# Optimization experiments

Hardware: AMD Instinct MI355X
Metric: run time of the kernel (lower is better)

## Reference

```python
import jax, jax.numpy as jnp
import numpy as np

B, C, H, W = 2, 64, 320, 640
TF = 16
HIDDEN = 48
HALF = 2
G = 8
D = 2 * HALF + 1
IN_CH = 2 * C + TF + 4 + G * D  # 164


def _sample_x(f, xs):
    # f: (B,C,H,W); xs: (B,H,W) absolute x sample coords.
    # Equivalent to F.grid_sample(align_corners=True, padding_mode='border')
    # with gy hitting exact integer rows -> pure 1D bilinear along W with border clamp.
    Wd = f.shape[-1]
    xs = jnp.clip(xs, 0.0, Wd - 1)
    x0 = jnp.floor(xs)
    w = (xs - x0)[:, None]                      # (B,1,H,W)
    i0 = x0.astype(jnp.int32)[:, None]          # (B,1,H,W)
    i1 = jnp.minimum(i0 + 1, Wd - 1)
    g0 = jnp.take_along_axis(f, jnp.broadcast_to(i0, f.shape), axis=3)
    g1 = jnp.take_along_axis(f, jnp.broadcast_to(i1, f.shape), axis=3)
    return g0 * (1.0 - w) + g1 * w


def _warp(fR, d):
    xx = jnp.arange(fR.shape[-1], dtype=fR.dtype)
    return _sample_x(fR, xx[None, None, :] - d[:, 0])


def _corr(fL, fR, d):
    b, c, h, w = fL.shape
    cg = c // G
    xx = jnp.arange(w, dtype=fL.dtype)
    fL_g = fL.reshape(b, G, cg, h, w)
    outs = []
    for i in range(D):  # small fixed D=5 loop over disparity offsets
        off = float(i - HALF)
        fR_w = _sample_x(fR, xx[None, None, :] - (d[:, 0] + off))
        outs.append((fL_g * fR_w.reshape(b, G, cg, h, w)).mean(axis=2))
    return jnp.stack(outs, axis=2).reshape(b, G * D, h, w)


def _conv(x, w, pad):
    return jax.lax.conv_general_dilated(x, w, (1, 1), ((pad, pad), (pad, pad)),
                                        dimension_numbers=('NCHW', 'OIHW', 'NCHW'))


def _gn(x, gamma, beta, groups=8, eps=1e-5):
    b, c, h, w = x.shape
    xg = x.reshape(b, groups, -1)
    m = xg.mean(axis=2, keepdims=True)
    v = ((xg - m) ** 2).mean(axis=2, keepdims=True)
    xg = (xg - m) * jax.lax.rsqrt(v + eps)
    return xg.reshape(b, c, h, w) * gamma[None, :, None, None] + beta[None, :, None, None]


def _head(h, w, b):
    return _conv(h, w, 0) + b[None, :, None, None]


def setup_inputs():
    key = jax.random.key(0)
    ks = jax.random.split(key, 32)
    inp = {}
    inp['d'] = jax.random.uniform(ks[0], (B, 1, H, W)) * 64.0
    inp['sx'] = jax.random.normal(ks[1], (B, 1, H, W)) * 0.1
    inp['sy'] = jax.random.normal(ks[2], (B, 1, H, W)) * 0.1
    inp['feat'] = jax.random.normal(ks[3], (B, TF, H, W))
    inp['conf'] = jax.random.uniform(ks[4], (B, 1, H, W))
    inp['fL'] = jax.random.normal(ks[5], (B, C, H, W))
    inp['fR'] = jax.random.normal(ks[6], (B, C, H, W))

    def cw(k, o, i, s):
        return jax.random.normal(k, (o, i, s, s)) * (1.0 / np.sqrt(i * s * s))

    inp['conv1_w'] = cw(ks[7], HIDDEN, IN_CH, 3)
    inp['conv2_w'] = cw(ks[8], HIDDEN, HIDDEN, 3)
    inp['conv3_w'] = cw(ks[9], HIDDEN, HIDDEN, 3)
    for j, nm in enumerate(['gn1', 'gn2', 'gn3']):
        inp[nm + '_g'] = 1.0 + 0.1 * jax.random.normal(ks[10 + 2 * j], (HIDDEN,))
        inp[nm + '_b'] = 0.1 * jax.random.normal(ks[11 + 2 * j], (HIDDEN,))
    inp['hd_w'] = cw(ks[16], 1, HIDDEN, 1); inp['hd_b'] = 0.01 * jax.random.normal(ks[17], (1,))
    inp['hsx_w'] = cw(ks[18], 1, HIDDEN, 1); inp['hsx_b'] = 0.01 * jax.random.normal(ks[19], (1,))
    inp['hsy_w'] = cw(ks[20], 1, HIDDEN, 1); inp['hsy_b'] = 0.01 * jax.random.normal(ks[21], (1,))
    inp['hc_w'] = cw(ks[22], 1, HIDDEN, 1); inp['hc_b'] = 0.01 * jax.random.normal(ks[23], (1,))
    inp['hf_w'] = cw(ks[24], TF, HIDDEN, 1); inp['hf_b'] = 0.01 * jax.random.normal(ks[25], (TF,))
    return inp


def reference(d, sx, sy, feat, conf, fL, fR,
              conv1_w, conv2_w, conv3_w,
              gn1_g, gn1_b, gn2_g, gn2_b, gn3_g, gn3_b,
              hd_w, hd_b, hsx_w, hsx_b, hsy_w, hsy_b, hc_w, hc_b, hf_w, hf_b):
    fR_w = _warp(fR, d)                               # standard warp (slope_aware off)
    cost = _corr(fL, fR, d)                           # (B, G*D, H, W)
    x = jnp.concatenate([fL, fR_w, feat, d, sx, sy, conf, cost], axis=1)
    h = jax.nn.silu(_gn(_conv(x, conv1_w, 1), gn1_g, gn1_b))
    h = jax.nn.silu(_gn(_conv(h, conv2_w, 1), gn2_g, gn2_b))
    h = jax.nn.silu(_gn(_conv(h, conv3_w, 1), gn3_g, gn3_b))
    d_out = jax.nn.softplus(_head(h, hd_w, hd_b) + d)  # gate == 1.0
    sx_out = sx + _head(h, hsx_w, hsx_b) * 0.1
    sy_out = sy + _head(h, hsy_w, hsy_b) * 0.1
    conf_out = jax.nn.sigmoid(_head(h, hc_w, hc_b) + 2.0 * conf - 1.0)
    feat_out = feat + _head(h, hf_w, hf_b)
    return (d_out, sx_out, sy_out, feat_out, conf_out)
```

## Files before the change

### kernel.cpp

```cpp
#include <hip/hip_runtime.h>
#include <hip/hip_bf16.h>

typedef __hip_bfloat16 bf16;
typedef unsigned short u16;
typedef short v8s __attribute__((ext_vector_type(8)));
typedef u16   v8u __attribute__((ext_vector_type(8)));
typedef float v4f __attribute__((ext_vector_type(4)));

#define Hd 320
#define Wd 640
#define HWP (Hd*Wd)
#define Bn 2
#define NCH1 188
#define HID 48
#define NBHW (Bn*HWP)
#define CP 40
#define NPIX 324
#define NSLAB 13

static __device__ __forceinline__ float b2f(bf16 v){ return __bfloat162float(v); }
static __device__ __forceinline__ bf16  f2b(float v){ return __float2bfloat16(v); }
static __device__ __forceinline__ u16 f2u(float v){ bf16 t = f2b(v); return *reinterpret_cast<u16*>(&t); }
static __device__ __forceinline__ float u2f(u16 u){ return __uint_as_float(((unsigned)u) << 16); }

template<typename T> static __device__ __forceinline__ float ld(const T* p, long i);
template<> __device__ __forceinline__ float ld<bf16>(const bf16* p, long i){ return b2f(p[i]); }
template<> __device__ __forceinline__ float ld<float>(const float* p, long i){ return p[i]; }
template<typename T> static __device__ __forceinline__ void stv(T* p, long i, float v);
template<> __device__ __forceinline__ void stv<bf16>(bf16* p, long i, float v){ p[i] = f2b(v); }
template<> __device__ __forceinline__ void stv<float>(float* p, long i, float v){ p[i] = v; }
template<typename T> struct want_flag;
template<> struct want_flag<bf16>  { static const int v = 0; };
template<> struct want_flag<float> { static const int v = 1; };

__global__ void probe_k(const u16* __restrict__ dq, int* __restrict__ flag)
{
  __shared__ int cnt;
  if (threadIdx.x == 0) cnt = 0;
  __syncthreads();
  int bad = 0;
  for (int i = threadIdx.x; i < 2048; i += 256) {
    float v = __uint_as_float(((unsigned)dq[2*i]) << 16);
    if (!(fabsf(v) <= 65.f)) bad++;
  }
  atomicAdd(&cnt, bad);
  __syncthreads();
  if (threadIdx.x == 0) *flag = (cnt > 64) ? 1 : 0;
}

static __device__ __forceinline__ int pack2orig(int p)
{
  if (p < 128) return p;
  if (p < 168) { int idx = p - 128; int i5 = idx >> 3, g = idx & 7; return 148 + g*5 + i5; }
  if (p < 184) return 128 + (p - 168);
  if (p < 188) return 144 + (p - 184);
  return -1;
}

template<typename T>
__global__ void wconv_k(const int* __restrict__ flag,
                        const T* __restrict__ c1, const T* __restrict__ c2,
                        const T* __restrict__ c3,
                        const T* __restrict__ hdw, const T* __restrict__ hdb,
                        const T* __restrict__ hsxw, const T* __restrict__ hsxb,
                        const T* __restrict__ hsyw, const T* __restrict__ hsyb,
                        const T* __restrict__ hcw,  const T* __restrict__ hcb,
                        const T* __restrict__ hfw,  const T* __restrict__ hfb,
                        u16* __restrict__ wf1, u16* __restrict__ wf2,
                        u16* __restrict__ wf3, float* __restrict__ wh,
                        float* __restrict__ bh)
{
  if (*flag != want_flag<T>::v) return;
  int stride = gridDim.x * blockDim.x;
  int t0 = blockIdx.x * blockDim.x + threadIdx.x;
  const int N1 = 6*9*3*64*8;
  for (int idx = t0; idx < N1; idx += stride) {
    int j = idx & 7; int lane = (idx >> 3) & 63; int rest = idx >> 9;
    int nt = rest % 3; rest /= 3; int tap = rest % 9; int chunk = rest / 9;
    int oc = nt*16 + (lane & 15);
    int cin = pack2orig(chunk*32 + (lane >> 4)*8 + j);
    float v = (cin >= 0) ? ld(c1, ((long)oc*NCH1 + cin)*9 + tap) : 0.f;
    wf1[idx] = f2u(v);
  }
  const int N2 = 2*9*3*64*8;
  for (int idx = t0; idx < N2; idx += stride) {
    int j = idx & 7; int lane = (idx >> 3) & 63; int rest = idx >> 9;
    int nt = rest % 3; rest /= 3; int tap = rest % 9; int chunk = rest / 9;
    int oc = nt*16 + (lane & 15);
    int cin = chunk*32 + (lane >> 4)*8 + j;
    float v2 = 0.f, v3 = 0.f;
    if (cin < HID) {
      v2 = ld(c2, ((long)oc*HID + cin)*9 + tap);
      v3 = ld(c3, ((long)oc*HID + cin)*9 + tap);
    }
    wf2[idx] = f2u(v2);
    wf3[idx] = f2u(v3);
  }
  for (int i = t0; i < HID; i += stride) {
    wh[0*HID + i] = ld(hdw, i);
    wh[1*HID + i] = ld(hsxw, i);
    wh[2*HID + i] = ld(hsyw, i);
    wh[3*HID + i] = ld(hcw, i);
  }
  for (int i = t0; i < 16*HID; i += stride) wh[4*HID + i] = ld(hfw, i);
  if (t0 == 0) {
    bh[0] = ld(hdb,0); bh[1] = ld(hsxb,0); bh[2] = ld(hsyb,0); bh[3] = ld(hcb,0);
    for (int j = 0; j < 16; ++j) bh[4+j] = ld(hfb, j);
  }
}

template<typename T>
__global__ __launch_bounds__(640) void build_x_k(
    const int* __restrict__ flag, int b,
    const T* __restrict__ dP,
    const T* __restrict__ fL, const T* __restrict__ fR,
    u16* __restrict__ xpk)
{
  if (*flag != want_flag<T>::v) return;
  __shared__ float rowR[8][Wd];
  int y = blockIdx.x;
  int x = threadIdx.x;
  long rowoff = (long)y*Wd;
  long pix = rowoff + x;
  float dval = ld(dP, (long)b*HWP + pix);
  float base = (float)x - dval;
  float i0f = floorf(base);
  float w = base - i0f;
  int i0b = (int)i0f;
  int idx0 = min(max(i0b - 2, 0), Wd-1);
  int idx1 = min(max(i0b - 1, 0), Wd-1);
  int idx2 = min(max(i0b    , 0), Wd-1);
  int idx3 = min(max(i0b + 1, 0), Wd-1);
  int idx4 = min(max(i0b + 2, 0), Wd-1);
  int idx5 = min(max(i0b + 3, 0), Wd-1);
  v8u cv0, cv1, cv2, cv3, cv4;

  #pragma unroll
  for (int g = 0; g < 8; ++g) {
    __syncthreads();
    #pragma unroll
    for (int cc = 0; cc < 8; ++cc)
      rowR[cc][x] = ld(fR, ((long)(b*64 + g*8 + cc))*HWP + rowoff + x);
    __syncthreads();
    v8u fwv;
    float a0=0.f, a1=0.f, a2=0.f, a3=0.f, a4=0.f;
    #pragma unroll
    for (int cc = 0; cc < 8; ++cc) {
      float fl = ld(fL, ((long)(b*64 + g*8 + cc))*HWP + pix);
      const float* rr = rowR[cc];
      float r0 = rr[idx0], r1 = rr[idx1], r2 = rr[idx2];
      float r3 = rr[idx3], r4 = rr[idx4], r5 = rr[idx5];
      float s0 = r4 + w*(r5 - r4);
      float s1 = r3 + w*(r4 - r3);
      float s2v = r2 + w*(r3 - r2);
      float s3 = r1 + w*(r2 - r1);
      float s4 = r0 + w*(r1 - r0);
      a0 += fl*s0; a1 += fl*s1; a2 += fl*s2v; a3 += fl*s3; a4 += fl*s4;
      fwv[cc] = f2u(s2v);
    }
    __builtin_nontemporal_store(fwv, (v8u*)&xpk[((long)g*HWP + pix)*8]);
    cv0[g] = f2u(a0*0.125f);
    cv1[g] = f2u(a1*0.125f);
    cv2[g] = f2u(a2*0.125f);
    cv3[g] = f2u(a3*0.125f);
    cv4[g] = f2u(a4*0.125f);
  }
  __builtin_nontemporal_store(cv0, (v8u*)&xpk[((long) 8*HWP + pix)*8]);
  __builtin_nontemporal_store(cv1, (v8u*)&xpk[((long) 9*HWP + pix)*8]);
  __builtin_nontemporal_store(cv2, (v8u*)&xpk[((long)10*HWP + pix)*8]);
  __builtin_nontemporal_store(cv3, (v8u*)&xpk[((long)11*HWP + pix)*8]);
  __builtin_nontemporal_store(cv4, (v8u*)&xpk[((long)12*HWP + pix)*8]);
}

static __device__ __forceinline__ void conv_epilogue(
    v4f (*acc)[3], u16* lds, float (*sred)[2], u16* out48,
    float* st, int b, int x0, int y0, int tid)
{
  int lane = tid & 63, wave = tid >> 6;
  #pragma unroll
  for (int nt = 0; nt < 3; ++nt) {
    float s = 0.f, s2 = 0.f;
    #pragma unroll
    for (int mi = 0; mi < 4; ++mi)
      #pragma unroll
      for (int r = 0; r < 4; ++r) { float v = acc[mi][nt][r]; s += v; s2 += v*v; }
    s  += __shfl_xor(s, 16);  s2 += __shfl_xor(s2, 16);
    s  += __shfl_xor(s, 32);  s2 += __shfl_xor(s2, 32);
    if (lane < 16) {
      int g = (nt*16 + lane) / 6;
      atomicAdd(&sred[g][0], s);
      atomicAdd(&sred[g][1], s2);
    }
  }
  __syncthreads();
  #pragma unroll
  for (int mi = 0; mi < 4; ++mi) {
    int py = wave*4 + mi;
    #pragma unroll
    for (int nt = 0; nt < 3; ++nt) {
      int oc = nt*16 + (lane & 15);
      #pragma unroll
      for (int r = 0; r < 4; ++r) {
        int px = (lane >> 4)*4 + r;
        lds[oc*270 + py*16 + px] = f2u(acc[mi][nt][r]);
      }
    }
  }
  __syncthreads();
  {
    int pix = tid;
    long base = ((long)(y0 + (pix>>4))*Wd + (x0 + (pix&15)))*HID;
    #pragma unroll
    for (int k = 0; k < 6; ++k) {
      v8u o;
      #pragma unroll
      for (int jj = 0; jj < 8; ++jj) o[jj] = lds[(k*8 + jj)*270 + pix];
      *(v8u*)&out48[base + k*8] = o;
    }
  }
  if (tid < 16) atomicAdd(&st[(b*8 + (tid>>1))*2 + (tid&1)], sred[tid>>1][tid&1]);
}

template<typename T>
__global__ __launch_bounds__(256) void conv1m_k(
    const int* __restrict__ flag, int b,
    const T* __restrict__ fL, const T* __restrict__ featP,
    const T* __restrict__ dP, const T* __restrict__ sxP, const T* __restrict__ syP,
    const T* __restrict__ confP,
    const u16* __restrict__ xpk, const u16* __restrict__ wfrag,
    u16* __restrict__ out48, float* __restrict__ st)
{
  if (*flag != want_flag<T>::v) return;
  __shared__ __attribute__((aligned(16))) u16 lds[12960];
  __shared__ float sred[8][2];
  int x0 = blockIdx.x*16, y0 = blockIdx.y*16;
  int tid = threadIdx.x, lane = tid & 63, wave = tid >> 6;
  if (tid < 16) ((float*)sred)[tid] = 0.f;
  const T* fLb = fL + (long)b*64*HWP;
  v4f acc[4][3];
  #pragma unroll
  for (int mi = 0; mi < 4; ++mi)
    #pragma unroll
    for (int nt = 0; nt < 3; ++nt) acc[mi][nt] = (v4f){0.f,0.f,0.f,0.f};

  for (int ch = 0; ch < 6; ++ch) {
    __syncthreads();
    for (int j = tid; j < 4*NPIX; j += 256) {
      int pix = j >> 2, q = j & 3;
      int r = pix / 18, cl = pix - r*18;
      int gy = y0 - 1 + r, gx = x0 - 1 + cl;
      bool inb = ((unsigned)gy < Hd) & ((unsigned)gx < Wd);
      long rowb = (long)gy*Wd + gx;
      v8u vals = {0,0,0,0,0,0,0,0};
      if (inb) {
        if (ch < 2) {
          int c0 = ch*32 + q*8;
          #pragma unroll
          for (int jj = 0; jj < 8; ++jj)
            vals[jj] = f2u(ld(fLb, (long)(c0+jj)*HWP + rowb));
        } else if (ch < 4) {
          vals = *(const v8u*)&xpk[((long)((ch-2)*4 + q)*HWP + rowb)*8];
        } else if (ch == 4) {
          vals = *(const v8u*)&xpk[((long)(8 + q)*HWP + rowb)*8];
        } else {
          if (q == 0) {
            vals = *(const v8u*)&xpk[((long)12*HWP + rowb)*8];
          } else if (q < 3) {
            #pragma unroll
            for (int jj = 0; jj < 8; ++jj)
              vals[jj] = f2u(ld(featP, ((long)(b*16 + (q-1)*8 + jj))*HWP + rowb));
          } else {
            vals[0] = f2u(ld(dP,   (long)b*HWP + rowb));
            vals[1] = f2u(ld(sxP,  (long)b*HWP + rowb));
            vals[2] = f2u(ld(syP,  (long)b*HWP + rowb));
            vals[3] = f2u(ld(confP,(long)b*HWP + rowb));
          }
        }
      }
      *(v8u*)&lds[pix*CP + q*8] = vals;
    }
    __syncthreads();
    #pragma unroll
    for (int tap = 0; tap < 9; ++tap) {
      int dr = tap / 3, dc = tap - dr*3;
      v8s bf0 = *(const v8s*)&wfrag[((((ch*9+tap)*3 + 0)*64 + lane) << 3)];
      v8s bf1 = *(const v8s*)&wfrag[((((ch*9+tap)*3 + 1)*64 + lane) << 3)];
      v8s bf2 = *(const v8s*)&wfrag[((((ch*9+tap)*3 + 2)*64 + lane) << 3)];
      #pragma unroll
      for (int mi = 0; mi < 4; ++mi) {
        int py = wave*4 + mi;
        const v8s a = *(const v8s*)&lds[((py+dr)*18 + (lane&15) + dc)*CP + (lane>>4)*8];
        acc[mi][0] = __builtin_amdgcn_mfma_f32_16x16x32_bf16(a, bf0, acc[mi][0], 0, 0, 0);
        acc[mi][1] = __builtin_amdgcn_mfma_f32_16x16x32_bf16(a, bf1, acc[mi][1], 0, 0, 0);
        acc[mi][2] = __builtin_amdgcn_mfma_f32_16x16x32_bf16(a, bf2, acc[mi][2], 0, 0, 0);
      }
    }
  }
  __syncthreads();
  conv_epilogue(acc, lds, sred, out48, st, b, x0, y0, tid);
}

template<typename T>
__global__ __launch_bounds__(256) void convHm_k(
    const int* __restrict__ flag, int b,
    const u16* __restrict__ in48, const u16* __restrict__ wfrag,
    const float* __restrict__ stats, const T* __restrict__ gamma,
    const T* __restrict__ beta, u16* __restrict__ out48, float* __restrict__ st)
{
  if (*flag != want_flag<T>::v) return;
  __shared__ __attribute__((aligned(16))) u16 lds[12960];
  __shared__ float sred[8][2];
  __shared__ float sc[HID], of[HID];
  int x0 = blockIdx.x*16, y0 = blockIdx.y*16;
  int tid = threadIdx.x, lane = tid & 63, wave = tid >> 6;
  if (tid < 16) ((float*)sred)[tid] = 0.f;
  if (tid < HID) {
    int g = tid / 6;
    const float inv_n = 1.f / (6.f * HWP);
    float s  = stats[(b*8+g)*2+0];
    float s2 = stats[(b*8+g)*2+1];
    float m  = s * inv_n;
    float var = s2 * inv_n - m*m;
    float rs = rsqrtf(fmaxf(var, 0.f) + 1e-5f);
    float gm = ld(gamma, tid), bt = ld(beta, tid);
    sc[tid] = rs * gm;
    of[tid] = bt - m * rs * gm;
  }
  v4f acc[4][3];
  #pragma unroll
  for (int mi = 0; mi < 4; ++mi)
    #pragma unroll
    for (int nt = 0; nt < 3; ++nt) acc[mi][nt] = (v4f){0.f,0.f,0.f,0.f};

  for (int ch = 0; ch < 2; ++ch) {
    int cb = ch*32;
    __syncthreads();
    for (int j = tid; j < 4*NPIX; j += 256) {
      int pix = j >> 2, q = j & 3;
      int r = pix / 18, cl = pix - r*18;
      int gy = y0 - 1 + r, gx = x0 - 1 + cl;
      int c0 = cb + q*8;
      v8u vals = {0,0,0,0,0,0,0,0};
      if ((((unsigned)gy < Hd) & ((unsigned)gx < Wd)) && c0 < HID) {
        v8u raw = *(const v8u*)&in48[((long)gy*Wd + gx)*HID + c0];
        #pragma unroll
        for (int jj = 0; jj < 8; ++jj) {
          float v = u2f(raw[jj]) * sc[c0+jj] + of[c0+jj];
          vals[jj] = f2u(v / (1.f + __expf(-v)));
        }
      }
      *(v8u*)&lds[pix*CP + q*8] = vals;
    }
    __syncthreads();
    #pragma unroll
    for (int tap = 0; tap < 9; ++tap) {
      int dr = tap / 3, dc = tap - dr*3;
      v8s bf0 = *(const v8s*)&wfrag[((((ch*9+tap)*3 + 0)*64 + lane) << 3)];
      v8s bf1 = *(const v8s*)&wfrag[((((ch*9+tap)*3 + 1)*64 + lane) << 3)];
      v8s bf2 = *(const v8s*)&wfrag[((((ch*9+tap)*3 + 2)*64 + lane) << 3)];
      #pragma unroll
      for (int mi = 0; mi < 4; ++mi) {
        int py = wave*4 + mi;
        const v8s a = *(const v8s*)&lds[((py+dr)*18 + (lane&15) + dc)*CP + (lane>>4)*8];
        acc[mi][0] = __builtin_amdgcn_mfma_f32_16x16x32_bf16(a, bf0, acc[mi][0], 0, 0, 0);
        acc[mi][1] = __builtin_amdgcn_mfma_f32_16x16x32_bf16(a, bf1, acc[mi][1], 0, 0, 0);
        acc[mi][2] = __builtin_amdgcn_mfma_f32_16x16x32_bf16(a, bf2, acc[mi][2], 0, 0, 0);
      }
    }
  }
  __syncthreads();
  conv_epilogue(acc, lds, sred, out48, st, b, x0, y0, tid);
}

template<typename T>
__global__ __launch_bounds__(256) void heads_k(
    const int* __restrict__ flag, int b,
    const u16* __restrict__ h48, const float* __restrict__ st,
    const T* __restrict__ gamma, const T* __restrict__ beta,
    const float* __restrict__ wh, const float* __restrict__ bh,
    const T* __restrict__ dP, const T* __restrict__ sxP, const T* __restrict__ syP,
    const T* __restrict__ featP, const T* __restrict__ confP,
    T* __restrict__ out)
{
  if (*flag != want_flag<T>::v) return;
  __shared__ float sc[HID], of[HID];
  int p = blockIdx.x * 256 + threadIdx.x;
  long idx = (long)b*HWP + p;
  if (threadIdx.x < HID) {
    int c = threadIdx.x;
    int g = c / 6;
    const float inv_n = 1.f / (6.f * HWP);
    float s  = st[(b*8+g)*2+0];
    float s2 = st[(b*8+g)*2+1];
    float m  = s * inv_n;
    float var = s2 * inv_n - m*m;
    float rs = rsqrtf(fmaxf(var, 0.f) + 1e-5f);
    float gm = ld(gamma, c), bt = ld(beta, c);
    sc[c] = rs * gm;
    of[c] = bt - m * rs * gm;
  }
  __syncthreads();
  float hv[HID];
  #pragma unroll
  for (int k = 0; k < 6; ++k) {
    v8u h8 = *(const v8u*)&h48[(long)p*HID + k*8];
    #pragma unroll
    for (int jj = 0; jj < 8; ++jj) {
      int c = k*8 + jj;
      float v = u2f(h8[jj]) * sc[c] + of[c];
      hv[c] = v / (1.f + __expf(-v));
    }
  }
  float dot[20];
  #pragma unroll
  for (int r = 0; r < 20; ++r) {
    float a = bh[r];
    #pragma unroll
    for (int c = 0; c < HID; ++c) a += wh[r*HID + c] * hv[c];
    dot[r] = a;
  }
  float dval = ld(dP, idx);
  float xd = dot[0] + dval;
  float sp = fmaxf(xd, 0.f) + log1pf(__expf(-fabsf(xd)));
  stv(out, idx, sp);
  stv(out, NBHW + idx,    ld(sxP, idx) + 0.1f*dot[1]);
  stv(out, 2L*NBHW + idx, ld(syP, idx) + 0.1f*dot[2]);
  float cf = dot[3] + 2.f*ld(confP, idx) - 1.f;
  stv(out, 19L*NBHW + idx, 1.f/(1.f + __expf(-cf)));
  #pragma unroll
  for (int r = 0; r < 16; ++r) {
    long fi = ((long)(b*16 + r))*HWP + p;
    stv(out, 3L*NBHW + fi, ld(featP, fi) + dot[4+r]);
  }
}

extern "C" void kernel_launch(void* const* d_in, const int* in_sizes, int n_in,
                              void* d_out, int out_size, void* d_ws, size_t ws_size,
                              hipStream_t stream)
{
  char* ws = (char*)d_ws;
  size_t off = 0;
  u16* xpk = (u16*)(ws + off); off += (size_t)NSLAB*HWP*8*sizeof(u16);
  u16* h1  = (u16*)(ws + off); off += (size_t)HID*HWP*sizeof(u16);
  u16* wf1 = (u16*)(ws + off); off += (size_t)6*9*3*64*8*sizeof(u16);
  u16* wf2 = (u16*)(ws + off); off += (size_t)2*9*3*64*8*sizeof(u16);
  u16* wf3 = (u16*)(ws + off); off += (size_t)2*9*3*64*8*sizeof(u16);
  float* wh = (float*)(ws + off); off += (size_t)20*HID*sizeof(float);
  float* bh = (float*)(ws + off); off += 32*sizeof(float);
  float* st = (float*)(ws + off); off += 96*sizeof(float);
  int* flag = (int*)(ws + off);   off += sizeof(int);
  u16* h2 = xpk;
  u16* h3 = h1;

  hipMemsetAsync(st, 0, 96*sizeof(float), stream);
  probe_k<<<1, 256, 0, stream>>>((const u16*)d_in[0], flag);

  dim3 cgrid(Wd/16, Hd/16, 1);

  #define LAUNCH_ALL(T) do { \
    const T* dP    = (const T*)d_in[0]; \
    const T* sxP   = (const T*)d_in[1]; \
    const T* syP   = (const T*)d_in[2]; \
    const T* featP = (const T*)d_in[3]; \
    const T* confP = (const T*)d_in[4]; \
    const T* fL    = (const T*)d_in[5]; \
    const T* fR    = (const T*)d_in[6]; \
    wconv_k<T><<<320, 256, 0, stream>>>(flag, (const T*)d_in[7], (const T*)d_in[8], \
        (const T*)d_in[9], (const T*)d_in[16], (const T*)d_in[17], (const T*)d_in[18], \
        (const T*)d_in[19], (const T*)d_in[20], (const T*)d_in[21], (const T*)d_in[22], \
        (const T*)d_in[23], (const T*)d_in[24], (const T*)d_in[25], wf1, wf2, wf3, wh, bh); \
    for (int b = 0; b < Bn; ++b) { \
      build_x_k<T><<<Hd, 640, 0, stream>>>(flag, b, dP, fL, fR, xpk); \
      conv1m_k<T><<<cgrid, 256, 0, stream>>>(flag, b, fL, featP, dP, sxP, syP, confP, xpk, wf1, h1, st + 0); \
      convHm_k<T><<<cgrid, 256, 0, stream>>>(flag, b, h1, wf2, st + 0,  (const T*)d_in[10], (const T*)d_in[11], h2, st + 32); \
      convHm_k<T><<<cgrid, 256, 0, stream>>>(flag, b, h2, wf3, st + 32, (const T*)d_in[12], (const T*)d_in[13], h3, st + 64); \
      heads_k<T><<<HWP/256, 256, 0, stream>>>(flag, b, h3, st + 64, (const T*)d_in[14], (const T*)d_in[15], \
          wh, bh, dP, sxP, syP, featP, confP, (T*)d_out); \
    } \
  } while (0)

  LAUNCH_ALL(bf16);
  LAUNCH_ALL(float);
  #undef LAUNCH_ALL
}
```

Measured before the change: 879.8 us.

## Pack fL into xpk slabs and register-prefetch next channel chunk in convs

build_x_k now also writes fL as packed bf16 slabs (NSLAB grows to 21), so conv1 reads only packed 8-channel vectors instead of eight strided planar loads per pixel. Both conv kernels restructure the staging loop so the next channel chunk's global loads are issued into registers before the MFMA loop on the current chunk, then written to LDS afterward. This overlaps global latency with compute at the cost of extra registers, an extra slab of writes in build_x, and additional barriers.

```diff
diff --git a/kernel.cpp b/kernel.cpp
--- a/kernel.cpp
+++ b/kernel.cpp
@@ -16,7 +16,7 @@
 #define NBHW (Bn*HWP)
 #define CP 40
 #define NPIX 324
-#define NSLAB 13
+#define NSLAB 21
 
 static __device__ __forceinline__ float b2f(bf16 v){ return __bfloat162float(v); }
 static __device__ __forceinline__ bf16  f2b(float v){ return __float2bfloat16(v); }
@@ -142,11 +142,12 @@
     for (int cc = 0; cc < 8; ++cc)
       rowR[cc][x] = ld(fR, ((long)(b*64 + g*8 + cc))*HWP + rowoff + x);
     __syncthreads();
-    v8u fwv;
+    v8u flv, fwv;
     float a0=0.f, a1=0.f, a2=0.f, a3=0.f, a4=0.f;
     #pragma unroll
     for (int cc = 0; cc < 8; ++cc) {
       float fl = ld(fL, ((long)(b*64 + g*8 + cc))*HWP + pix);
+      flv[cc] = f2u(fl);
       const float* rr = rowR[cc];
       float r0 = rr[idx0], r1 = rr[idx1], r2 = rr[idx2];
       float r3 = rr[idx3], r4 = rr[idx4], r5 = rr[idx5];
@@ -158,18 +159,19 @@
       a0 += fl*s0; a1 += fl*s1; a2 += fl*s2v; a3 += fl*s3; a4 += fl*s4;
       fwv[cc] = f2u(s2v);
     }
-    __builtin_nontemporal_store(fwv, (v8u*)&xpk[((long)g*HWP + pix)*8]);
+    __builtin_nontemporal_store(flv, (v8u*)&xpk[((long)g*HWP + pix)*8]);
+    __builtin_nontemporal_store(fwv, (v8u*)&xpk[((long)(8 + g)*HWP + pix)*8]);
     cv0[g] = f2u(a0*0.125f);
     cv1[g] = f2u(a1*0.125f);
     cv2[g] = f2u(a2*0.125f);
     cv3[g] = f2u(a3*0.125f);
     cv4[g] = f2u(a4*0.125f);
   }
-  __builtin_nontemporal_store(cv0, (v8u*)&xpk[((long) 8*HWP + pix)*8]);
-  __builtin_nontemporal_store(cv1, (v8u*)&xpk[((long) 9*HWP + pix)*8]);
-  __builtin_nontemporal_store(cv2, (v8u*)&xpk[((long)10*HWP + pix)*8]);
-  __builtin_nontemporal_store(cv3, (v8u*)&xpk[((long)11*HWP + pix)*8]);
-  __builtin_nontemporal_store(cv4, (v8u*)&xpk[((long)12*HWP + pix)*8]);
+  __builtin_nontemporal_store(cv0, (v8u*)&xpk[((long)16*HWP + pix)*8]);
+  __builtin_nontemporal_store(cv1, (v8u*)&xpk[((long)17*HWP + pix)*8]);
+  __builtin_nontemporal_store(cv2, (v8u*)&xpk[((long)18*HWP + pix)*8]);
+  __builtin_nontemporal_store(cv3, (v8u*)&xpk[((long)19*HWP + pix)*8]);
+  __builtin_nontemporal_store(cv4, (v8u*)&xpk[((long)20*HWP + pix)*8]);
 }
 
 static __device__ __forceinline__ void conv_epilogue(
@@ -224,7 +226,7 @@
 template<typename T>
 __global__ __launch_bounds__(256) void conv1m_k(
     const int* __restrict__ flag, int b,
-    const T* __restrict__ fL, const T* __restrict__ featP,
+    const T* __restrict__ featP,
     const T* __restrict__ dP, const T* __restrict__ sxP, const T* __restrict__ syP,
     const T* __restrict__ confP,
     const u16* __restrict__ xpk, const u16* __restrict__ wfrag,
@@ -236,50 +238,69 @@
   int x0 = blockIdx.x*16, y0 = blockIdx.y*16;
   int tid = threadIdx.x, lane = tid & 63, wave = tid >> 6;
   if (tid < 16) ((float*)sred)[tid] = 0.f;
-  const T* fLb = fL + (long)b*64*HWP;
   v4f acc[4][3];
   #pragma unroll
   for (int mi = 0; mi < 4; ++mi)
     #pragma unroll
     for (int nt = 0; nt < 3; ++nt) acc[mi][nt] = (v4f){0.f,0.f,0.f,0.f};
 
-  for (int ch = 0; ch < 6; ++ch) {
-    __syncthreads();
-    for (int j = tid; j < 4*NPIX; j += 256) {
+  #pragma unroll
+  for (int k = 0; k < 6; ++k) {
+    int j = tid + k*256;
+    if (j < 4*NPIX) {
       int pix = j >> 2, q = j & 3;
       int r = pix / 18, cl = pix - r*18;
       int gy = y0 - 1 + r, gx = x0 - 1 + cl;
-      bool inb = ((unsigned)gy < Hd) & ((unsigned)gx < Wd);
-      long rowb = (long)gy*Wd + gx;
       v8u vals = {0,0,0,0,0,0,0,0};
-      if (inb) {
-        if (ch < 2) {
-          int c0 = ch*32 + q*8;
-          #pragma unroll
-          for (int jj = 0; jj < 8; ++jj)
-            vals[jj] = f2u(ld(fLb, (long)(c0+jj)*HWP + rowb));
-        } else if (ch < 4) {
-          vals = *(const v8u*)&xpk[((long)((ch-2)*4 + q)*HWP + rowb)*8];
-        } else if (ch == 4) {
-          vals = *(const v8u*)&xpk[((long)(8 + q)*HWP + rowb)*8];
-        } else {
-          if (q == 0) {
-            vals = *(const v8u*)&xpk[((long)12*HWP + rowb)*8];
-          } else if (q < 3) {
-            #pragma unroll
-            for (int jj = 0; jj < 8; ++jj)
-              vals[jj] = f2u(ld(featP, ((long)(b*16 + (q-1)*8 + jj))*HWP + rowb));
-          } else {
-            vals[0] = f2u(ld(dP,   (long)b*HWP + rowb));
-            vals[1] = f2u(ld(sxP,  (long)b*HWP + rowb));
-            vals[2] = f2u(ld(syP,  (long)b*HWP + rowb));
-            vals[3] = f2u(ld(confP,(long)b*HWP + rowb));
-          }
-        }
-      }
+      if (((unsigned)gy < Hd) & ((unsigned)gx < Wd))
+        vals = *(const v8u*)&xpk[((long)q*HWP + (long)gy*Wd + gx)*8];
       *(v8u*)&lds[pix*CP + q*8] = vals;
     }
+  }
+
+  v8u pf0, pf1, pf2, pf3, pf4, pf5;
+
+#define PF_LOAD(k, dst) do { \
+    dst = (v8u){0,0,0,0,0,0,0,0}; \
+    int j = tid + k*256; \
+    if (j < 4*NPIX) { \
+      int pix = j >> 2, q = j & 3; \
+      int r = pix / 18, cl = pix - r*18; \
+      int gy = y0 - 1 + r, gx = x0 - 1 + cl; \
+      if ((((unsigned)gy < Hd) & ((unsigned)gx < Wd)) && (nch < 5 || q == 0)) \
+        dst = *(const v8u*)&xpk[((long)(nch < 5 ? nch*4 + q : 20)*HWP + (long)gy*Wd + gx)*8]; \
+    } } while (0)
+
+#define PF_WRITE(k, src) do { \
+    int j = tid + k*256; \
+    if (j < 4*NPIX) { \
+      int pix = j >> 2, q = j & 3; \
+      int r = pix / 18, cl = pix - r*18; \
+      int gy = y0 - 1 + r, gx = x0 - 1 + cl; \
+      bool inb = ((unsigned)gy < Hd) & ((unsigned)gx < Wd); \
+      long rowb = (long)gy*Wd + gx; \
+      v8u vals = src; \
+      if (nch == 5 && inb) { \
+        if (q == 1 || q == 2) { \
+          _Pragma("unroll") \
+          for (int jj = 0; jj < 8; ++jj) \
+            vals[jj] = f2u(ld(featP, ((long)(b*16 + (q-1)*8 + jj))*HWP + rowb)); \
+        } else if (q == 3) { \
+          vals[0] = f2u(ld(dP,   (long)b*HWP + rowb)); \
+          vals[1] = f2u(ld(sxP,  (long)b*HWP + rowb)); \
+          vals[2] = f2u(ld(syP,  (long)b*HWP + rowb)); \
+          vals[3] = f2u(ld(confP,(long)b*HWP + rowb)); \
+        } } \
+      *(v8u*)&lds[pix*CP + q*8] = vals; \
+    } } while (0)
+
+  for (int ch = 0; ch < 6; ++ch) {
+    int nch = ch + 1;
     __syncthreads();
+    if (nch < 6) {
+      PF_LOAD(0, pf0); PF_LOAD(1, pf1); PF_LOAD(2, pf2);
+      PF_LOAD(3, pf3); PF_LOAD(4, pf4); PF_LOAD(5, pf5);
+    }
     #pragma unroll
     for (int tap = 0; tap < 9; ++tap) {
       int dr = tap / 3, dc = tap - dr*3;
@@ -295,8 +316,14 @@
         acc[mi][2] = __builtin_amdgcn_mfma_f32_16x16x32_bf16(a, bf2, acc[mi][2], 0, 0, 0);
       }
     }
-  }
-  __syncthreads();
+    __syncthreads();
+    if (nch < 6) {
+      PF_WRITE(0, pf0); PF_WRITE(1, pf1); PF_WRITE(2, pf2);
+      PF_WRITE(3, pf3); PF_WRITE(4, pf4); PF_WRITE(5, pf5);
+    }
+  }
+#undef PF_LOAD
+#undef PF_WRITE
   conv_epilogue(acc, lds, sred, out48, st, b, x0, y0, tid);
 }
 
@@ -332,42 +359,70 @@
     #pragma unroll
     for (int nt = 0; nt < 3; ++nt) acc[mi][nt] = (v4f){0.f,0.f,0.f,0.f};
 
-  for (int ch = 0; ch < 2; ++ch) {
-    int cb = ch*32;
-    __syncthreads();
-    for (int j = tid; j < 4*NPIX; j += 256) {
-      int pix = j >> 2, q = j & 3;
-      int r = pix / 18, cl = pix - r*18;
-      int gy = y0 - 1 + r, gx = x0 - 1 + cl;
-      int c0 = cb + q*8;
-      v8u vals = {0,0,0,0,0,0,0,0};
-      if ((((unsigned)gy < Hd) & ((unsigned)gx < Wd)) && c0 < HID) {
-        v8u raw = *(const v8u*)&in48[((long)gy*Wd + gx)*HID + c0];
-        #pragma unroll
-        for (int jj = 0; jj < 8; ++jj) {
-          float v = u2f(raw[jj]) * sc[c0+jj] + of[c0+jj];
-          vals[jj] = f2u(v / (1.f + __expf(-v)));
-        }
-      }
-      *(v8u*)&lds[pix*CP + q*8] = vals;
-    }
-    __syncthreads();
-    #pragma unroll
-    for (int tap = 0; tap < 9; ++tap) {
-      int dr = tap / 3, dc = tap - dr*3;
-      v8s bf0 = *(const v8s*)&wfrag[((((ch*9+tap)*3 + 0)*64 + lane) << 3)];
-      v8s bf1 = *(const v8s*)&wfrag[((((ch*9+tap)*3 + 1)*64 + lane) << 3)];
-      v8s bf2 = *(const v8s*)&wfrag[((((ch*9+tap)*3 + 2)*64 + lane) << 3)];
-      #pragma unroll
-      for (int mi = 0; mi < 4; ++mi) {
-        int py = wave*4 + mi;
-        const v8s a = *(const v8s*)&lds[((py+dr)*18 + (lane&15) + dc)*CP + (lane>>4)*8];
-        acc[mi][0] = __builtin_amdgcn_mfma_f32_16x16x32_bf16(a, bf0, acc[mi][0], 0, 0, 0);
-        acc[mi][1] = __builtin_amdgcn_mfma_f32_16x16x32_bf16(a, bf1, acc[mi][1], 0, 0, 0);
-        acc[mi][2] = __builtin_amdgcn_mfma_f32_16x16x32_bf16(a, bf2, acc[mi][2], 0, 0, 0);
-      }
-    }
-  }
+  v8u pf0, pf1, pf2, pf3, pf4, pf5;
+
+#define HPF_LOAD(k, dst, cb) do { \
+    dst = (v8u){0,0,0,0,0,0,0,0}; \
+    int j = tid + k*256; \
+    if (j < 4*NPIX) { \
+      int pix = j >> 2, q = j & 3; \
+      int r = pix / 18, cl = pix - r*18; \
+      int gy = y0 - 1 + r, gx = x0 - 1 + cl; \
+      int c0 = (cb) + q*8; \
+      if ((((unsigned)gy < Hd) & ((unsigned)gx < Wd)) && c0 < HID) \
+        dst = *(const v8u*)&in48[((long)gy*Wd + gx)*HID + c0]; \
+    } } while (0)
+
+#define HPF_WRITE(k, src, cb) do { \
+    int j = tid + k*256; \
+    if (j < 4*NPIX) { \
+      int pix = j >> 2, q = j & 3; \
+      int r = pix / 18, cl = pix - r*18; \
+      int gy = y0 - 1 + r, gx = x0 - 1 + cl; \
+      int c0 = (cb) + q*8; \
+      v8u vals = {0,0,0,0,0,0,0,0}; \
+      if ((((unsigned)gy < Hd) & ((unsigned)gx < Wd)) && c0 < HID) { \
+        _Pragma("unroll") \
+        for (int jj = 0; jj < 8; ++jj) { \
+          float v = u2f(src[jj]) * sc[c0+jj] + of[c0+jj]; \
+          vals[jj] = f2u(v / (1.f + __expf(-v))); \
+        } } \
+      *(v8u*)&lds[pix*CP + q*8] = vals; \
+    } } while (0)
+
+#define HMFMA(ch) do { \
+    _Pragma("unroll") \
+    for (int tap = 0; tap < 9; ++tap) { \
+      int dr = tap / 3, dc = tap - dr*3; \
+      v8s bf0 = *(const v8s*)&wfrag[(((((ch)*9+tap)*3 + 0)*64 + lane) << 3)]; \
+      v8s bf1 = *(const v8s*)&wfrag[(((((ch)*9+tap)*3 + 1)*64 + lane) << 3)]; \
+      v8s bf2 = *(const v8s*)&wfrag[(((((ch)*9+tap)*3 + 2)*64 + lane) << 3)]; \
+      _Pragma("unroll") \
+      for (int mi = 0; mi < 4; ++mi) { \
+        int py = wave*4 + mi; \
+        const v8s a = *(const v8s*)&lds[((py+dr)*18 + (lane&15) + dc)*CP + (lane>>4)*8]; \
+        acc[mi][0] = __builtin_amdgcn_mfma_f32_16x16x32_bf16(a, bf0, acc[mi][0], 0, 0, 0); \
+        acc[mi][1] = __builtin_amdgcn_mfma_f32_16x16x32_bf16(a, bf1, acc[mi][1], 0, 0, 0); \
+        acc[mi][2] = __builtin_amdgcn_mfma_f32_16x16x32_bf16(a, bf2, acc[mi][2], 0, 0, 0); \
+      } } } while (0)
+
+  HPF_LOAD(0, pf0, 0); HPF_LOAD(1, pf1, 0); HPF_LOAD(2, pf2, 0);
+  HPF_LOAD(3, pf3, 0); HPF_LOAD(4, pf4, 0); HPF_LOAD(5, pf5, 0);
+  __syncthreads();
+  HPF_WRITE(0, pf0, 0); HPF_WRITE(1, pf1, 0); HPF_WRITE(2, pf2, 0);
+  HPF_WRITE(3, pf3, 0); HPF_WRITE(4, pf4, 0); HPF_WRITE(5, pf5, 0);
+  HPF_LOAD(0, pf0, 32); HPF_LOAD(1, pf1, 32); HPF_LOAD(2, pf2, 32);
+  HPF_LOAD(3, pf3, 32); HPF_LOAD(4, pf4, 32); HPF_LOAD(5, pf5, 32);
+  __syncthreads();
+  HMFMA(0);
+  __syncthreads();
+  HPF_WRITE(0, pf0, 32); HPF_WRITE(1, pf1, 32); HPF_WRITE(2, pf2, 32);
+  HPF_WRITE(3, pf3, 32); HPF_WRITE(4, pf4, 32); HPF_WRITE(5, pf5, 32);
+  __syncthreads();
+  HMFMA(1);
+#undef HPF_LOAD
+#undef HPF_WRITE
+#undef HMFMA
   __syncthreads();
   conv_epilogue(acc, lds, sred, out48, st, b, x0, y0, tid);
 }
@@ -471,7 +526,7 @@
         (const T*)d_in[23], (const T*)d_in[24], (const T*)d_in[25], wf1, wf2, wf3, wh, bh); \
     for (int b = 0; b < Bn; ++b) { \
       build_x_k<T><<<Hd, 640, 0, stream>>>(flag, b, dP, fL, fR, xpk); \
-      conv1m_k<T><<<cgrid, 256, 0, stream>>>(flag, b, fL, featP, dP, sxP, syP, confP, xpk, wf1, h1, st + 0); \
+      conv1m_k<T><<<cgrid, 256, 0, stream>>>(flag, b, featP, dP, sxP, syP, confP, xpk, wf1, h1, st + 0); \
       convHm_k<T><<<cgrid, 256, 0, stream>>>(flag, b, h1, wf2, st + 0,  (const T*)d_in[10], (const T*)d_in[11], h2, st + 32); \
       convHm_k<T><<<cgrid, 256, 0, stream>>>(flag, b, h2, wf3, st + 32, (const T*)d_in[12], (const T*)d_in[13], h3, st + 64); \
       heads_k<T><<<HWP/256, 256, 0, stream>>>(flag, b, h3, st + 64, (const T*)d_in[14], (const T*)d_in[15], \
```

Result: faster. 847.3 us (-3.7%).
